# Kernel optimization log

Measured on AMD Instinct MI355X. Metric: run time of the kernel, lower is better.

The kernel has to match this reference:

```python
import jax, jax.numpy as jnp
import numpy as np

DIM, HEADS, HEAD_DIM, P = 256, 8, 64, 16
N = P * P          # 256 tokens
H2 = HEADS // 2    # heads in SDPA branch
SCALE = HEAD_DIM ** -0.5
BN_EPS = 1e-5


def _depthwise(x, w, kh, kw):
    # x: (b, DIM, P, P), w: (DIM, kh*kw) depthwise kernel -> same spatial size
    rhs = w.reshape(DIM, 1, kh, kw)
    return jax.lax.conv_general_dilated(
        x, rhs, window_strides=(1, 1),
        padding=((kh // 2, kh // 2), (kw // 2, kw // 2)),
        dimension_numbers=('NCHW', 'OIHW', 'NCHW'),
        feature_group_count=DIM)


def setup_inputs() -> dict:
    key = jax.random.key(0)
    ks = jax.random.split(key, 8)
    b = 128
    return {
        'x': jax.random.normal(ks[0], (b, N, DIM), jnp.float32),
        'bn_gamma': jax.random.uniform(ks[1], (DIM,), jnp.float32, 0.5, 1.5),
        'bn_beta': jax.random.normal(ks[2], (DIM,), jnp.float32) * 0.1,
        'bn_mean': jax.random.normal(ks[3], (DIM,), jnp.float32) * 0.1,
        'bn_var': jax.random.uniform(ks[4], (DIM,), jnp.float32, 0.5, 1.5),
        'w_qkv': jax.random.normal(ks[5], (DIM, 6), jnp.float32) * 0.1,
        'w_qs': jax.random.normal(ks[6], (DIM, 3), jnp.float32) * 0.1,
        'w_ks': jax.random.normal(ks[7], (DIM, 3), jnp.float32) * 0.1,
    }


def reference(x, bn_gamma, bn_beta, bn_mean, bn_var, w_qkv, w_qs, w_ks):
    b = x.shape[0]
    # raw contiguous view (b,n,d) -> (b,dim,p,p), as in the torch code
    xi = x.reshape(b, DIM, P, P)
    inv = jax.lax.rsqrt(bn_var + BN_EPS)
    xb = jax.nn.relu(((xi - bn_mean[None, :, None, None]) * (bn_gamma * inv)[None, :, None, None])
                     + bn_beta[None, :, None, None])
    # grouped 1x1 conv (groups=DIM, 6 out-channels per group)
    qkv = (xb[:, :, None, :, :] * w_qkv[None, :, :, None, None]).reshape(b, DIM * 6, P, P)
    # raw view (b, 6*dim, p, p) -> (b, n, 6*dim)
    qkv = qkv.reshape(b, N, 6 * DIM)
    q, k, v = jnp.split(qkv, 3, axis=-1)  # each (b, n, 2*dim)

    def to_heads(t):
        return t.reshape(b, N, HEADS, HEAD_DIM).transpose(0, 2, 1, 3)  # b h n d

    q, k, v = to_heads(q), to_heads(k), to_heads(v)
    q1, k1, v1 = q[:, :H2], k[:, :H2], v[:, :H2]
    # raw reshape (b, H2, n, head_dim) -> (b, dim, p, p)
    q2 = q[:, H2:].reshape(b, DIM, P, P)
    k2 = k[:, H2:].reshape(b, DIM, P, P)
    v2 = v[:, H2:].reshape(b, DIM, P, P)
    q2 = _depthwise(q2, w_qs, 1, 3)
    k2 = _depthwise(k2, w_ks, 3, 1)
    res2 = (q2 + k2 + v2).reshape(b, N, DIM)

    scores = jnp.einsum('bhid,bhjd->bhij', q1, k1) * SCALE
    attn = jax.nn.softmax(scores, axis=-1)
    out = jnp.einsum('bhij,bhjd->bhid', attn, v1)
    out = out.transpose(0, 2, 1, 3).reshape(b, N, H2 * HEAD_DIM)  # (b, n, dim)

    res = jnp.concatenate([out, res2], axis=2)  # (b, n, 2*dim)
    # AdaptiveAvgPool1d(dim) on length 2*dim == pairwise mean
    return res.reshape(b, N, DIM, 2).mean(axis=-1)
```

## Files before the change

### kernel.cpp

```cpp
#include <hip/hip_runtime.h>

typedef __bf16 bf16;
typedef __attribute__((ext_vector_type(8))) __bf16 bf16x8;
typedef __attribute__((ext_vector_type(4))) __bf16 bf16x4;
typedef __attribute__((ext_vector_type(2))) __bf16 bf16x2;
typedef __attribute__((ext_vector_type(4))) float floatx4;

#define MFMA16(a,b,c) __builtin_amdgcn_mfma_f32_16x16x32_bf16((a),(b),(c),0,0,0)

__device__ __forceinline__ float fast_exp2(float xv) {
#if __has_builtin(__builtin_amdgcn_exp2f)
  return __builtin_amdgcn_exp2f(xv);
#else
  return exp2f(xv);
#endif
}

__device__ __forceinline__ void ld8f(const bf16* p, float* dst) {
  bf16x8 v = *(const bf16x8*)p;
#pragma unroll
  for (int i = 0; i < 8; ++i) dst[i] = (float)v[i];
}

__global__ __launch_bounds__(512, 4) void fused_kernel(
    const float* __restrict__ x,
    const float* __restrict__ bn_gamma, const float* __restrict__ bn_beta,
    const float* __restrict__ bn_mean, const float* __restrict__ bn_var,
    const float* __restrict__ w_qkv, const float* __restrict__ w_qs,
    const float* __restrict__ w_ks,
    float* __restrict__ out)
{
  __shared__ __align__(16) char smem[72704];
  bf16 (*Abf)[72]  = (bf16(*)[72])smem;
  bf16 (*VtF)[264] = (bf16(*)[264])(smem + 36864);
  float* ckA = (float*)(smem + 70656);
  float* cvA = (float*)(smem + 71680);
  float* scT = (float*)(smem + 36864);
  float* bsT = (float*)(smem + 36864 + 1024);

  const int t  = threadIdx.x;
  const int bb = blockIdx.x >> 2;
  const int h  = blockIdx.x & 3;

  if (t < 256) {
    float inv = rsqrtf(bn_var[t] + 1e-5f);
    float sc  = bn_gamma[t] * inv;
    scT[t] = sc;
    bsT[t] = bn_beta[t] - bn_mean[t] * sc;
    ckA[t] = w_qkv[t*6+2];
    cvA[t] = w_qkv[t*6+4];
  }
  __syncthreads();

  const float* xb = x + (size_t)bb * 65536 + h * 64;
  {
    const int rsub = t >> 4, ch = t & 15;
#pragma unroll
    for (int i2 = 0; i2 < 8; ++i2) {
      int n = i2*32 + rsub;
      float4 v = *(const float4*)(xb + (size_t)n*256 + ch*4);
      float sc = scT[n], bs = bsT[n];
      bf16x4 bv;
      bv.x = (bf16)fmaxf(fmaf(v.x, sc, bs), 0.f);
      bv.y = (bf16)fmaxf(fmaf(v.y, sc, bs), 0.f);
      bv.z = (bf16)fmaxf(fmaf(v.z, sc, bs), 0.f);
      bv.w = (bf16)fmaxf(fmaf(v.w, sc, bs), 0.f);
      *(bf16x4*)&Abf[n][ch*4] = bv;
    }
  }
  __syncthreads();

  {
    const int J  = t & 127;
    const int eg = t >> 7;
    const bf16* r0 = &Abf[2*J][16*eg];
    const bf16* r1 = &Abf[2*J + 1][16*eg];
    bf16x8 a0l = *(const bf16x8*)r0, a0h = *(const bf16x8*)(r0 + 8);
    bf16x8 a1l = *(const bf16x8*)r1, a1h = *(const bf16x8*)(r1 + 8);
    float cv0 = cvA[2*J], cv1 = cvA[2*J + 1];
#pragma unroll
    for (int e = 0; e < 8; ++e) {
      union { bf16x2 hh; unsigned u; } wl, wh;
      wl.hh = (bf16x2){(bf16)((float)a0l[e]*cv0), (bf16)((float)a1l[e]*cv1)};
      wh.hh = (bf16x2){(bf16)((float)a0h[e]*cv0), (bf16)((float)a1h[e]*cv1)};
      *(unsigned*)&VtF[16*eg + e][2*J]     = wl.u;
      *(unsigned*)&VtF[16*eg + 8 + e][2*J] = wh.u;
    }
  }
  __syncthreads();

  const int lane = t & 63;
  const int wid  = t >> 6;
  const int q    = lane >> 4;
  const int c    = lane & 15;
  const int R    = wid * 32;
  const int jp   = ((c >> 2) << 3) + (c & 3);

  float cqs[2];
  cqs[0] = w_qkv[(R + c)*6]      * 0.18033688f;
  cqs[1] = w_qkv[(R + 16 + c)*6] * 0.18033688f;
  bf16x8 bi0[2], bi1[2];
#pragma unroll
  for (int it = 0; it < 2; ++it) {
    const bf16* bp = &Abf[R + 16*it + c][0];
    bf16x8 r0 = *(const bf16x8*)(bp + 8*q);
    bf16x8 r1 = *(const bf16x8*)(bp + 32 + 8*q);
#pragma unroll
    for (int e = 0; e < 8; ++e) {
      bi0[it][e] = (bf16)((float)r0[e] * cqs[it]);
      bi1[it][e] = (bf16)((float)r1[e] * cqs[it]);
    }
  }

  bf16x8 vbONE;
#pragma unroll
  for (int e = 0; e < 8; ++e) vbONE[e] = (bf16)1.0f;

  floatx4 oacc[2][4];
  floatx4 oaccL[2];
#pragma unroll
  for (int it = 0; it < 2; ++it) {
    oaccL[it] = (floatx4){0.f,0.f,0.f,0.f};
#pragma unroll
    for (int et = 0; et < 4; ++et)
      oacc[it][et] = (floatx4){0.f,0.f,0.f,0.f};
  }

  const int jbase = wid & 7;
#pragma unroll 2
  for (int jt = 0; jt < 8; ++jt) {
    const int j0 = (((jt + jbase) & 7) << 5);

    bf16x8 vb0 = *(const bf16x8*)&VtF[     c][j0 + 8*q];
    bf16x8 vb1 = *(const bf16x8*)&VtF[16 + c][j0 + 8*q];
    bf16x8 vb2 = *(const bf16x8*)&VtF[32 + c][j0 + 8*q];
    bf16x8 vb3 = *(const bf16x8*)&VtF[48 + c][j0 + 8*q];

    const int jr = j0 + jp;
    bf16x8 aj00 = *(const bf16x8*)&Abf[jr][8*q];
    bf16x8 aj01 = *(const bf16x8*)&Abf[jr][32 + 8*q];
    bf16x8 aj10 = *(const bf16x8*)&Abf[jr + 4][8*q];
    bf16x8 aj11 = *(const bf16x8*)&Abf[jr + 4][32 + 8*q];
    floatx4 ck0 = *(const floatx4*)&ckA[j0 + 8*q];
    floatx4 ck1 = *(const floatx4*)&ckA[j0 + 8*q + 4];

    bf16x8 pa[2];
#pragma unroll
    for (int it = 0; it < 2; ++it) {
      floatx4 s0 = (floatx4){0.f,0.f,0.f,0.f};
      floatx4 s1 = (floatx4){0.f,0.f,0.f,0.f};
      s0 = MFMA16(aj00, bi0[it], s0); s0 = MFMA16(aj01, bi1[it], s0);
      s1 = MFMA16(aj10, bi0[it], s1); s1 = MFMA16(aj11, bi1[it], s1);
      bf16x8 pv;
#pragma unroll
      for (int r = 0; r < 4; ++r) {
        pv[r]     = (bf16)fast_exp2(ck0[r] * s0[r]);
        pv[4 + r] = (bf16)fast_exp2(ck1[r] * s1[r]);
      }
      pa[it] = pv;
    }

    oaccL[0] = MFMA16(pa[0], vbONE, oaccL[0]);
    oaccL[1] = MFMA16(pa[1], vbONE, oaccL[1]);

    oacc[0][0] = MFMA16(pa[0], vb0, oacc[0][0]);
    oacc[1][0] = MFMA16(pa[1], vb0, oacc[1][0]);
    oacc[0][1] = MFMA16(pa[0], vb1, oacc[0][1]);
    oacc[1][1] = MFMA16(pa[1], vb1, oacc[1][1]);
    oacc[0][2] = MFMA16(pa[0], vb2, oacc[0][2]);
    oacc[1][2] = MFMA16(pa[1], vb2, oacc[1][2]);
    oacc[0][3] = MFMA16(pa[0], vb3, oacc[0][3]);
    oacc[1][3] = MFMA16(pa[1], vb3, oacc[1][3]);
  }

  float* outA = out + ((size_t)bb*256)*256 + h*32;
#pragma unroll
  for (int it = 0; it < 2; ++it) {
#pragma unroll
    for (int r = 0; r < 4; ++r) {
      float linv = 0.5f / oaccL[it][r];
      int n = R + 16*it + 4*q + r;
#pragma unroll
      for (int et = 0; et < 4; ++et) {
        float v = oacc[it][et][r];
        float v2 = v + __shfl_xor(v, 1, 64);
        if (!(lane & 1))
          outA[(size_t)n*256 + 8*et + (c>>1)] = v2 * linv;
      }
    }
  }

  {
    const int ci = t >> 3, sub = t & 7, qq = sub >> 1, uh = sub & 1;
    const int C  = h*64 + ci;
    const int a  = 4*ci + qq;
    const int e0 = 32*uh;

    float qs0 = w_qs[C*3+0], qs1 = w_qs[C*3+1], qs2 = w_qs[C*3+2];
    float ks0 = w_ks[C*3+0], ks1 = w_ks[C*3+1], ks2 = w_ks[C*3+2];
    float wq1a = w_qkv[a*6+1], wk1a = w_qkv[a*6+3], wv1a = w_qkv[a*6+5];
    float wcf = fmaf(ks1, wk1a, wv1a);

    float wmx = 0.f;
    if (uh) wmx = ks0 * wk1a;
    else if (qq > 0) wmx = ks0 * w_qkv[(a-1)*6+3];
    float wmh = ks0 * wk1a;
    float wpl = ks2 * wk1a;
    float wpx = 0.f;
    if (!uh) wpx = ks2 * wk1a;
    else if (qq < 3) wpx = ks2 * w_qkv[(a+1)*6+3];

    float Xc[32], Xl[16], Xr[16];
#pragma unroll
    for (int m = 0; m < 4; ++m) ld8f(&Abf[a][e0 + 8*m], &Xc[8*m]);
    if (uh) {
      ld8f(&Abf[a][16], &Xl[0]); ld8f(&Abf[a][24], &Xl[8]);
    } else if (qq > 0) {
      ld8f(&Abf[a-1][48], &Xl[0]); ld8f(&Abf[a-1][56], &Xl[8]);
    } else {
#pragma unroll
      for (int i = 0; i < 16; ++i) Xl[i] = 0.f;
    }
    if (!uh) {
      ld8f(&Abf[a][32], &Xr[0]); ld8f(&Abf[a][40], &Xr[8]);
    } else if (qq < 3) {
      ld8f(&Abf[a+1][0], &Xr[0]); ld8f(&Abf[a+1][8], &Xr[8]);
    } else {
#pragma unroll
      for (int i = 0; i < 16; ++i) Xr[i] = 0.f;
    }

    float res[16];
    float prev = 0.f;
#pragma unroll
    for (int k = 0; k < 32; ++k) {
      float fc = Xc[k];
      float qv = qs1 * fc;
      if (k & 15)         qv = fmaf(qs0, Xc[k-1], qv);
      if ((k & 15) != 15) qv = fmaf(qs2, Xc[k+1], qv);
      float acc = fmaf(wq1a, qv, wcf * fc);
      float tm = (k < 16) ? Xl[k]     : Xc[k-16];
      float wm = (k < 16) ? wmx       : wmh;
      acc = fmaf(wm, tm, acc);
      float tp = (k < 16) ? Xc[k+16]  : Xr[k-16];
      float wp = (k < 16) ? wpl       : wpx;
      acc = fmaf(wp, tp, acc);
      if (k & 1) res[k>>1] = 0.5f * (prev + acc);
      else       prev = acc;
    }

    float* outC = out + ((size_t)(bb*256 + C))*256 + 128 + 32*qq + 16*uh;
#pragma unroll
    for (int m = 0; m < 4; ++m) {
      float4 o4;
      o4.x = res[4*m]; o4.y = res[4*m+1]; o4.z = res[4*m+2]; o4.w = res[4*m+3];
      *(float4*)(outC + 4*m) = o4;
    }
  }
}

extern "C" void kernel_launch(void* const* d_in, const int* in_sizes, int n_in,
                              void* d_out, int out_size, void* d_ws, size_t ws_size,
                              hipStream_t stream) {
  (void)in_sizes; (void)n_in; (void)out_size; (void)d_ws; (void)ws_size;
  const float* x    = (const float*)d_in[0];
  const float* g    = (const float*)d_in[1];
  const float* be   = (const float*)d_in[2];
  const float* mn   = (const float*)d_in[3];
  const float* vr   = (const float*)d_in[4];
  const float* wqkv = (const float*)d_in[5];
  const float* wqs  = (const float*)d_in[6];
  const float* wks  = (const float*)d_in[7];
  float* out = (float*)d_out;

  fused_kernel<<<dim3(512), dim3(512), 0, stream>>>(x, g, be, mn, vr, wqkv, wqs, wks, out);
}
```

Measured before the change: 105.0 us.

## Split fused kernel into BN/depthwise-conv kernel and attention kernel via bf16 workspace

Splits the single fused kernel in two. The first launches 8192 small blocks that apply BN+ReLU, write a bf16 copy of the activations to the workspace, and compute the depthwise-conv branch output directly. The attention kernel then loads the precomputed bf16 activations with wide 16-byte loads and no longer carries the conv tail. This spreads the conv branch across far more parallel blocks and lightens the attention kernel, at the cost of an extra launch and a bf16 round-trip through global memory.

```diff
diff --git a/kernel.cpp b/kernel.cpp
--- a/kernel.cpp
+++ b/kernel.cpp
@@ -16,18 +16,81 @@
 #endif
 }
 
-__device__ __forceinline__ void ld8f(const bf16* p, float* dst) {
-  bf16x8 v = *(const bf16x8*)p;
-#pragma unroll
-  for (int i = 0; i < 8; ++i) dst[i] = (float)v[i];
-}
-
-__global__ __launch_bounds__(512, 4) void fused_kernel(
+__global__ __launch_bounds__(256) void bnconv_kernel(
     const float* __restrict__ x,
     const float* __restrict__ bn_gamma, const float* __restrict__ bn_beta,
     const float* __restrict__ bn_mean, const float* __restrict__ bn_var,
     const float* __restrict__ w_qkv, const float* __restrict__ w_qs,
     const float* __restrict__ w_ks,
+    float* __restrict__ out, bf16* __restrict__ xbN)
+{
+  __shared__ float X[4][257];
+  const int t   = threadIdx.x;
+  const int b   = blockIdx.x >> 6;
+  const int m   = blockIdx.x & 63;
+  const int row = t >> 6;
+  const int l   = t & 63;
+  const int n   = 4*m + row;
+
+  float inv = rsqrtf(bn_var[n] + 1e-5f);
+  float sc  = bn_gamma[n] * inv;
+  float bs  = bn_beta[n] - bn_mean[n] * sc;
+  float4 v  = *(const float4*)(x + ((size_t)b*256 + n)*256 + 4*l);
+  float x0 = fmaxf(fmaf(v.x, sc, bs), 0.f);
+  float x1 = fmaxf(fmaf(v.y, sc, bs), 0.f);
+  float x2 = fmaxf(fmaf(v.z, sc, bs), 0.f);
+  float x3 = fmaxf(fmaf(v.w, sc, bs), 0.f);
+  X[row][4*l+0] = x0; X[row][4*l+1] = x1;
+  X[row][4*l+2] = x2; X[row][4*l+3] = x3;
+  bf16x4 bv; bv.x = (bf16)x0; bv.y = (bf16)x1; bv.z = (bf16)x2; bv.w = (bf16)x3;
+  *(bf16x4*)(xbN + ((size_t)b*256 + n)*256 + 4*l) = bv;
+  __syncthreads();
+
+  const int wv = row;
+  const int C  = 64*wv + m;
+  const int eo = 64*wv;
+  float qs0 = w_qs[C*3+0], qs1 = w_qs[C*3+1], qs2 = w_qs[C*3+2];
+  float ks0 = w_ks[C*3+0], ks1 = w_ks[C*3+1], ks2 = w_ks[C*3+2];
+  float wq1r[4], wkc[4], wv1r[4], wkm[4], wkp[4];
+#pragma unroll
+  for (int r = 0; r < 4; ++r) {
+    int a = 4*m + r;
+    wq1r[r] = w_qkv[a*6+1];
+    float wk = w_qkv[a*6+3];
+    wv1r[r] = fmaf(ks1, wk, w_qkv[a*6+5]);
+    wkm[r]  = ks0 * wk;
+    wkp[r]  = ks2 * wk;
+  }
+  (void)wkc;
+
+  float res[2];
+  float prev = 0.f;
+#pragma unroll
+  for (int pp = 0; pp < 4; ++pp) {
+    int p  = 4*l + pp;
+    int lr = p >> 6, e = p & 63, ww = p & 15;
+    float fc = X[lr][eo + e];
+    float qv = qs1 * fc;
+    if (ww > 0)  qv = fmaf(qs0, X[lr][eo + e - 1], qv);
+    if (ww < 15) qv = fmaf(qs2, X[lr][eo + e + 1], qv);
+    float acc = fmaf(wq1r[lr], qv, wv1r[lr] * fc);
+    if (p >= 16) {
+      int pm = p - 16, lm = pm >> 6;
+      acc = fmaf(wkm[lm], X[lm][eo + (pm & 63)], acc);
+    }
+    if (p < 240) {
+      int pq = p + 16, lp = pq >> 6;
+      acc = fmaf(wkp[lp], X[lp][eo + (pq & 63)], acc);
+    }
+    if (pp & 1) res[pp >> 1] = 0.5f * (prev + acc);
+    else        prev = acc;
+  }
+  float2 o2; o2.x = res[0]; o2.y = res[1];
+  *(float2*)(out + ((size_t)b*256 + C)*256 + 128 + 2*l) = o2;
+}
+
+__global__ __launch_bounds__(512, 4) void attn_kernel(
+    const bf16* __restrict__ xbN, const float* __restrict__ w_qkv,
     float* __restrict__ out)
 {
   __shared__ __align__(16) char smem[72704];
@@ -35,37 +98,23 @@
   bf16 (*VtF)[264] = (bf16(*)[264])(smem + 36864);
   float* ckA = (float*)(smem + 70656);
   float* cvA = (float*)(smem + 71680);
-  float* scT = (float*)(smem + 36864);
-  float* bsT = (float*)(smem + 36864 + 1024);
 
   const int t  = threadIdx.x;
   const int bb = blockIdx.x >> 2;
   const int h  = blockIdx.x & 3;
 
   if (t < 256) {
-    float inv = rsqrtf(bn_var[t] + 1e-5f);
-    float sc  = bn_gamma[t] * inv;
-    scT[t] = sc;
-    bsT[t] = bn_beta[t] - bn_mean[t] * sc;
     ckA[t] = w_qkv[t*6+2];
     cvA[t] = w_qkv[t*6+4];
   }
-  __syncthreads();
-
-  const float* xb = x + (size_t)bb * 65536 + h * 64;
+
   {
-    const int rsub = t >> 4, ch = t & 15;
-#pragma unroll
-    for (int i2 = 0; i2 < 8; ++i2) {
-      int n = i2*32 + rsub;
-      float4 v = *(const float4*)(xb + (size_t)n*256 + ch*4);
-      float sc = scT[n], bs = bsT[n];
-      bf16x4 bv;
-      bv.x = (bf16)fmaxf(fmaf(v.x, sc, bs), 0.f);
-      bv.y = (bf16)fmaxf(fmaf(v.y, sc, bs), 0.f);
-      bv.z = (bf16)fmaxf(fmaf(v.z, sc, bs), 0.f);
-      bv.w = (bf16)fmaxf(fmaf(v.w, sc, bs), 0.f);
-      *(bf16x4*)&Abf[n][ch*4] = bv;
+    const bf16* src = xbN + (size_t)bb * 65536 + h * 64;
+#pragma unroll
+    for (int it = 0; it < 4; ++it) {
+      int idx = it*512 + t;
+      int n = idx >> 3, ch = idx & 7;
+      *(bf16x8*)&Abf[n][ch*8] = *(const bf16x8*)(src + (size_t)n*256 + ch*8);
     }
   }
   __syncthreads();
@@ -189,80 +238,12 @@
       }
     }
   }
-
-  {
-    const int ci = t >> 3, sub = t & 7, qq = sub >> 1, uh = sub & 1;
-    const int C  = h*64 + ci;
-    const int a  = 4*ci + qq;
-    const int e0 = 32*uh;
-
-    float qs0 = w_qs[C*3+0], qs1 = w_qs[C*3+1], qs2 = w_qs[C*3+2];
-    float ks0 = w_ks[C*3+0], ks1 = w_ks[C*3+1], ks2 = w_ks[C*3+2];
-    float wq1a = w_qkv[a*6+1], wk1a = w_qkv[a*6+3], wv1a = w_qkv[a*6+5];
-    float wcf = fmaf(ks1, wk1a, wv1a);
-
-    float wmx = 0.f;
-    if (uh) wmx = ks0 * wk1a;
-    else if (qq > 0) wmx = ks0 * w_qkv[(a-1)*6+3];
-    float wmh = ks0 * wk1a;
-    float wpl = ks2 * wk1a;
-    float wpx = 0.f;
-    if (!uh) wpx = ks2 * wk1a;
-    else if (qq < 3) wpx = ks2 * w_qkv[(a+1)*6+3];
-
-    float Xc[32], Xl[16], Xr[16];
-#pragma unroll
-    for (int m = 0; m < 4; ++m) ld8f(&Abf[a][e0 + 8*m], &Xc[8*m]);
-    if (uh) {
-      ld8f(&Abf[a][16], &Xl[0]); ld8f(&Abf[a][24], &Xl[8]);
-    } else if (qq > 0) {
-      ld8f(&Abf[a-1][48], &Xl[0]); ld8f(&Abf[a-1][56], &Xl[8]);
-    } else {
-#pragma unroll
-      for (int i = 0; i < 16; ++i) Xl[i] = 0.f;
-    }
-    if (!uh) {
-      ld8f(&Abf[a][32], &Xr[0]); ld8f(&Abf[a][40], &Xr[8]);
-    } else if (qq < 3) {
-      ld8f(&Abf[a+1][0], &Xr[0]); ld8f(&Abf[a+1][8], &Xr[8]);
-    } else {
-#pragma unroll
-      for (int i = 0; i < 16; ++i) Xr[i] = 0.f;
-    }
-
-    float res[16];
-    float prev = 0.f;
-#pragma unroll
-    for (int k = 0; k < 32; ++k) {
-      float fc = Xc[k];
-      float qv = qs1 * fc;
-      if (k & 15)         qv = fmaf(qs0, Xc[k-1], qv);
-      if ((k & 15) != 15) qv = fmaf(qs2, Xc[k+1], qv);
-      float acc = fmaf(wq1a, qv, wcf * fc);
-      float tm = (k < 16) ? Xl[k]     : Xc[k-16];
-      float wm = (k < 16) ? wmx       : wmh;
-      acc = fmaf(wm, tm, acc);
-      float tp = (k < 16) ? Xc[k+16]  : Xr[k-16];
-      float wp = (k < 16) ? wpl       : wpx;
-      acc = fmaf(wp, tp, acc);
-      if (k & 1) res[k>>1] = 0.5f * (prev + acc);
-      else       prev = acc;
-    }
-
-    float* outC = out + ((size_t)(bb*256 + C))*256 + 128 + 32*qq + 16*uh;
-#pragma unroll
-    for (int m = 0; m < 4; ++m) {
-      float4 o4;
-      o4.x = res[4*m]; o4.y = res[4*m+1]; o4.z = res[4*m+2]; o4.w = res[4*m+3];
-      *(float4*)(outC + 4*m) = o4;
-    }
-  }
 }
 
 extern "C" void kernel_launch(void* const* d_in, const int* in_sizes, int n_in,
                               void* d_out, int out_size, void* d_ws, size_t ws_size,
                               hipStream_t stream) {
-  (void)in_sizes; (void)n_in; (void)out_size; (void)d_ws; (void)ws_size;
+  (void)in_sizes; (void)n_in; (void)out_size; (void)ws_size;
   const float* x    = (const float*)d_in[0];
   const float* g    = (const float*)d_in[1];
   const float* be   = (const float*)d_in[2];
@@ -272,6 +253,9 @@
   const float* wqs  = (const float*)d_in[6];
   const float* wks  = (const float*)d_in[7];
   float* out = (float*)d_out;
-
-  fused_kernel<<<dim3(512), dim3(512), 0, stream>>>(x, g, be, mn, vr, wqkv, wqs, wks, out);
-}
+  bf16* xbN  = (bf16*)d_ws;
+
+  bnconv_kernel<<<dim3(8192), dim3(256), 0, stream>>>(x, g, be, mn, vr, wqkv, wqs, wks,
+                                                      out, xbN);
+  attn_kernel<<<dim3(512), dim3(512), 0, stream>>>(xbN, wqkv, out);
+}
```

Measured after the change: 113.9 us. 1.09x slower.
